# Kernel optimization log

Hardware: AMD Instinct MI355X
Metric: run time of the kernel (lower is better)

The kernel has to match this reference:

```python
import jax, jax.numpy as jnp
import numpy as np


def _xcorr3x3_valid(x, k):
    # x: [B,H,W], k: [B,3,3] per-sample kernel; cross-correlation (matches F.conv2d), VALID padding
    B, H, W = x.shape
    out = jnp.zeros((B, H - 2, W - 2), dtype=x.dtype)
    for u in range(3):
        for v in range(3):
            out = out + x[:, u:u + H - 2, v:v + W - 2] * k[:, u, v, None, None]
    return out


def setup_inputs() -> dict:
    key = jax.random.key(0)
    ks = jax.random.split(key, 4)
    B, H, W = 256, 256, 256
    pred = jax.random.normal(ks[0], (B, H, W), dtype=jnp.float32)
    rhs = jax.random.normal(ks[1], (B, H - 2, W - 2), dtype=jnp.float32)
    Laplace_kernel = jax.random.normal(ks[2], (B, 3, 3), dtype=jnp.float32)
    Df_dr_kernel = jax.random.normal(ks[3], (B, 3, 3), dtype=jnp.float32)
    # physically sensible meshgrids: R in [1,2] (avoids div-by-zero), Z in [-1,1]
    r = jnp.linspace(1.0, 2.0, W, dtype=jnp.float32)
    z = jnp.linspace(-1.0, 1.0, H, dtype=jnp.float32)
    RR = jnp.broadcast_to(r[None, None, :], (B, H, W)).astype(jnp.float32)
    ZZ = jnp.broadcast_to(z[None, :, None], (B, H, W)).astype(jnp.float32)
    Gauss_kernel = (jnp.array([[1., 2., 1.], [2., 4., 2.], [1., 2., 1.]], dtype=jnp.float32) / 16.0)
    return {"pred": pred, "rhs": rhs, "Laplace_kernel": Laplace_kernel,
            "Df_dr_kernel": Df_dr_kernel, "RR": RR, "ZZ": ZZ, "Gauss_kernel": Gauss_kernel}


def reference(pred, rhs, Laplace_kernel, Df_dr_kernel, RR, ZZ, Gauss_kernel):
    # Lpsi, Dpsi_dr: per-sample 3x3 VALID stencils -> [B, H-2, W-2]
    Lpsi = _xcorr3x3_valid(pred, Laplace_kernel)
    Dpsi_dr = -_xcorr3x3_valid(pred, Df_dr_kernel)
    Dpsi_dr = Dpsi_dr / RR[:, 1:-1, 1:-1]
    lhs = Lpsi - Dpsi_dr
    hr = (RR[:, 1, 2] - RR[:, 1, 1])[:, None, None]
    hz = (ZZ[:, 2, 1] - ZZ[:, 1, 1])[:, None, None]
    alfa = -2.0 * (hr ** 2 + hz ** 2)
    GS_ope = lhs * alfa / (hr ** 2 * hz ** 2)
    # Gaussian smoothing, shared kernel, SAME padding (cross-correlation; kernel is symmetric)
    sm = jax.lax.conv_general_dilated(
        GS_ope[:, None, :, :], Gauss_kernel[None, None, :, :],
        window_strides=(1, 1), padding='SAME')
    GS_ope_smooth = -sm
    rhs_computed = -GS_ope_smooth[:, 0, :, :]
    return jnp.mean((rhs_computed - rhs) ** 2)
```

## Files before the change

### kernel.cpp

```cpp
#include <hip/hip_runtime.h>


__global__ __launch_bounds__(256)
void pde_loss_kernel(const float* __restrict__ pred,
                     const float* __restrict__ rhs,
                     const float* __restrict__ KL,
                     const float* __restrict__ KD,
                     const float* __restrict__ RR,
                     const float* __restrict__ ZZ,
                     float* __restrict__ partials)
{
    constexpr int H = 256, W = 256, OH = 254, OW = 254, SR = 8;
    const int tid = threadIdx.x;
    const int l   = tid & 63;
    const int wv  = tid >> 6;
    const int b   = blockIdx.x >> 3;
    const int strip = (blockIdx.x & 7) * 4 + wv;
    const int o0 = strip * SR;
    const int o1 = (o0 + SR < OH) ? (o0 + SR) : OH;

    const size_t ib = (size_t)b * H * W;
    const float* predb = pred + ib;
    const float* rhsb  = rhs + (size_t)b * OH * OW;
    const int c0 = 4 * l;

    float4 p[12];
#pragma unroll
    for (int j = 0; j < 12; ++j) {
        const int row = o0 - 1 + j;
        p[j] = make_float4(0.f, 0.f, 0.f, 0.f);
        if ((unsigned)row < (unsigned)H)
            p[j] = *(const float4*)(predb + (size_t)row * W + c0);
    }
    float2 r0[8], r1[8];
#pragma unroll
    for (int j = 0; j < 8; ++j) {
        r0[j] = make_float2(0.f, 0.f); r1[j] = make_float2(0.f, 0.f);
        if (o0 + j < o1) {
            const float* rr = rhsb + (size_t)(o0 + j) * OW + c0;
            r0[j] = *(const float2*)rr;
            if (c0 + 2 < OW) r1[j] = *(const float2*)(rr + 2);
        }
    }

    const float hr  = RR[ib + W + 2] - RR[ib + W + 1];
    const float hz  = ZZ[ib + 2 * W + 1] - ZZ[ib + W + 1];
    float kl[9], kd[9];
#pragma unroll
    for (int t = 0; t < 9; ++t) {
        kl[t] = __int_as_float(__builtin_amdgcn_readfirstlane(__float_as_int(KL[b * 9 + t])));
        kd[t] = __int_as_float(__builtin_amdgcn_readfirstlane(__float_as_int(KD[b * 9 + t])));
    }
    float4 invr;
    invr.x = 1.0f / RR[ib + W + (c0 + 1)];
    invr.y = 1.0f / RR[ib + W + (c0 + 2)];
    invr.z = 1.0f / RR[ib + W + (c0 + 3)];
    invr.w = 1.0f / RR[ib + W + ((c0 + 4 < W) ? (c0 + 4) : (W - 1))];

    __builtin_amdgcn_sched_barrier(0);

    const float hr2 = hr * hr, hz2 = hz * hz;
    const float s   = -2.0f * (hr2 + hz2) / (hr2 * hz2);

    const float mzw = (l == 63) ? 0.f : 1.f;
    const float m23 = (c0 + 2 < OW) ? 1.f : 0.f;
    const float m0  = (l > 0) ? 1.f : 0.f;
    float4 s4, sir4;
    s4.x = s; s4.y = s; s4.z = s * mzw; s4.w = s * mzw;
    sir4.x = s4.x * invr.x; sir4.y = s4.y * invr.y;
    sir4.z = s4.z * invr.z; sir4.w = s4.w * invr.w;

#define SROW(SV, P, nx, ny, k0, k1, k2, KC)                                   \
    SV.x = fmaf(P.x, KC[k0], fmaf(P.y, KC[k1], fmaf(P.z, KC[k2], SV.x)));     \
    SV.y = fmaf(P.y, KC[k0], fmaf(P.z, KC[k1], fmaf(P.w, KC[k2], SV.y)));     \
    SV.z = fmaf(P.z, KC[k0], fmaf(P.w, KC[k1], fmaf(nx,  KC[k2], SV.z)));     \
    SV.w = fmaf(P.w, KC[k0], fmaf(nx,  KC[k1], fmaf(ny,  KC[k2], SV.w)));

    float ax = __shfl(p[0].x, l + 1, 64), ay = __shfl(p[0].y, l + 1, 64);
    float bx = __shfl(p[1].x, l + 1, 64), by = __shfl(p[1].y, l + 1, 64);
    float4 ghm2 = make_float4(0.f, 0.f, 0.f, 0.f);
    float4 ghm1 = make_float4(0.f, 0.f, 0.f, 0.f);
    float acc = 0.0f;

#pragma unroll
    for (int K = 0; K < 10; ++K) {
        const int g = o0 - 1 + K;

        const float cx = __shfl(p[K + 2].x, l + 1, 64);
        const float cy = __shfl(p[K + 2].y, l + 1, 64);

        float4 SL = make_float4(0.f, 0.f, 0.f, 0.f);
        float4 SD = make_float4(0.f, 0.f, 0.f, 0.f);
        if (g <= o1 && (unsigned)g < (unsigned)OH) {
            SROW(SL, p[K],     ax, ay, 0, 1, 2, kl)
            SROW(SL, p[K + 1], bx, by, 3, 4, 5, kl)
            SROW(SL, p[K + 2], cx, cy, 6, 7, 8, kl)
            SROW(SD, p[K],     ax, ay, 0, 1, 2, kd)
            SROW(SD, p[K + 1], bx, by, 3, 4, 5, kd)
            SROW(SD, p[K + 2], cx, cy, 6, 7, 8, kd)
        }
        float4 gs;
        gs.x = fmaf(s4.x, SL.x, sir4.x * SD.x);
        gs.y = fmaf(s4.y, SL.y, sir4.y * SD.y);
        gs.z = fmaf(s4.z, SL.z, sir4.z * SD.z);
        gs.w = fmaf(s4.w, SL.w, sir4.w * SD.w);

        const float up = __shfl(gs.w, l - 1, 64) * m0;
        const float dn = __shfl(gs.x, l + 1, 64);
        float4 gh;
        gh.x = fmaf(2.f, gs.x, up   + gs.y);
        gh.y = fmaf(2.f, gs.y, gs.x + gs.z);
        gh.z = fmaf(2.f, gs.z, gs.y + gs.w);
        gh.w = fmaf(2.f, gs.w, gs.z + dn);

        if (K >= 2) {
            const int i = g - 1;
            if (i < o1) {
                const float smx = (ghm2.x + 2.f * ghm1.x + gh.x) * 0.0625f;
                const float smy = (ghm2.y + 2.f * ghm1.y + gh.y) * 0.0625f;
                const float smz = (ghm2.z + 2.f * ghm1.z + gh.z) * 0.0625f;
                const float smw = (ghm2.w + 2.f * ghm1.w + gh.w) * 0.0625f;
                const float dx = smx - r0[K - 2].x;
                const float dy = smy - r0[K - 2].y;
                const float dz = (smz - r1[K - 2].x) * m23;
                const float dw = (smw - r1[K - 2].y) * m23;
                acc = fmaf(dx, dx, acc);
                acc = fmaf(dy, dy, acc);
                acc = fmaf(dz, dz, acc);
                acc = fmaf(dw, dw, acc);
            }
        }

        ghm2 = ghm1; ghm1 = gh;
        ax = bx; ay = by; bx = cx; by = cy;
    }
#undef SROW

#pragma unroll
    for (int off = 32; off > 0; off >>= 1)
        acc += __shfl_down(acc, off, 64);
    __shared__ float wsum[4];
    if (l == 0) wsum[wv] = acc;
    __syncthreads();
    if (tid == 0)
        partials[blockIdx.x] = (wsum[0] + wsum[1]) + (wsum[2] + wsum[3]);
}

__global__ __launch_bounds__(256)
void reduce_kernel(const float* __restrict__ partials, float* __restrict__ out,
                   int n, float inv_n)
{
    const int tid = threadIdx.x;
    float a = 0.0f;
    for (int i = tid; i < n; i += 256) a += partials[i];
#pragma unroll
    for (int off = 32; off > 0; off >>= 1)
        a += __shfl_down(a, off, 64);
    __shared__ float w[4];
    if ((tid & 63) == 0) w[tid >> 6] = a;
    __syncthreads();
    if (tid == 0) out[0] = ((w[0] + w[1]) + (w[2] + w[3])) * inv_n;
}

extern "C" void kernel_launch(void* const* d_in, const int* in_sizes, int n_in,
                              void* d_out, int out_size, void* d_ws, size_t ws_size,
                              hipStream_t stream) {
    const float* pred = (const float*)d_in[0];
    const float* rhs  = (const float*)d_in[1];
    const float* KL   = (const float*)d_in[2];
    const float* KD   = (const float*)d_in[3];
    const float* RR   = (const float*)d_in[4];
    const float* ZZ   = (const float*)d_in[5];
    float* out = (float*)d_out;

    const int B = in_sizes[2] / 9;
    const int nblocks = B * 8;
    const float inv_n = 1.0f / ((float)B * 254.0f * 254.0f);

    float* partials = (float*)d_ws;
    pde_loss_kernel<<<dim3(nblocks), dim3(256), 0, stream>>>(
        pred, rhs, KL, KD, RR, ZZ, partials);
    reduce_kernel<<<dim3(1), dim3(256), 0, stream>>>(partials, out, nblocks, inv_n);
}
```

Baseline: 221.1 us.

## Stage pred rows in LDS via direct global-to-LDS loads and fold stencil coefficients

Pred rows for the block are now loaded straight into shared memory with global_load_lds, and each wave reads its 12 rows from LDS. The right-halo columns come from an extra float2 LDS read, which replaces the cross-lane shuffles. The two per-sample stencils are also folded into one combined per-column coefficient set (klv*s + kdv*s/r). That halves the FMAs in the inner loop. The cost is a 37KB LDS footprint per block, which limits occupancy, plus a block barrier. The per-lane kernel coefficients also lose their scalar readfirstlane form and now occupy more VGPRs.

```diff
diff --git a/kernel.cpp b/kernel.cpp
--- a/kernel.cpp
+++ b/kernel.cpp
@@ -1,5 +1,12 @@
 #include <hip/hip_runtime.h>
 
+
+__device__ __forceinline__ void g2lds16(const float* g, float* l) {
+    __builtin_amdgcn_global_load_lds(
+        (const __attribute__((address_space(1))) void*)g,
+        (__attribute__((address_space(3))) void*)l,
+        16 , 0, 0);
+}
 
 __global__ __launch_bounds__(256)
 void pde_loss_kernel(const float* __restrict__ pred,
@@ -10,28 +17,23 @@
                      const float* __restrict__ ZZ,
                      float* __restrict__ partials)
 {
-    constexpr int H = 256, W = 256, OH = 254, OW = 254, SR = 8;
+    constexpr int H = 256, W = 256, OH = 254, OW = 254;
+    __shared__ float lds[36 * 256 + 16];
+    __shared__ float wsum[4];
+
     const int tid = threadIdx.x;
     const int l   = tid & 63;
     const int wv  = tid >> 6;
     const int b   = blockIdx.x >> 3;
-    const int strip = (blockIdx.x & 7) * 4 + wv;
-    const int o0 = strip * SR;
-    const int o1 = (o0 + SR < OH) ? (o0 + SR) : OH;
+    const int rb  = (blockIdx.x & 7) * 32;
+    const int o0  = rb + wv * 8;
+    const int o1  = (o0 + 8 < OH) ? (o0 + 8) : OH;
+    const int c0  = 4 * l;
 
     const size_t ib = (size_t)b * H * W;
     const float* predb = pred + ib;
     const float* rhsb  = rhs + (size_t)b * OH * OW;
-    const int c0 = 4 * l;
 
-    float4 p[12];
-#pragma unroll
-    for (int j = 0; j < 12; ++j) {
-        const int row = o0 - 1 + j;
-        p[j] = make_float4(0.f, 0.f, 0.f, 0.f);
-        if ((unsigned)row < (unsigned)H)
-            p[j] = *(const float4*)(predb + (size_t)row * W + c0);
-    }
     float2 r0[8], r1[8];
 #pragma unroll
     for (int j = 0; j < 8; ++j) {
@@ -42,68 +44,78 @@
             if (c0 + 2 < OW) r1[j] = *(const float2*)(rr + 2);
         }
     }
+    const float hr = RR[ib + W + 2] - RR[ib + W + 1];
+    const float hz = ZZ[ib + 2 * W + 1] - ZZ[ib + W + 1];
+    float klv[9], kdv[9];
+#pragma unroll
+    for (int t = 0; t < 9; ++t) { klv[t] = KL[b * 9 + t]; kdv[t] = KD[b * 9 + t]; }
+    float4 invr;
+    invr.x = RR[ib + W + (c0 + 1)];
+    invr.y = RR[ib + W + (c0 + 2)];
+    invr.z = RR[ib + W + (c0 + 3)];
+    invr.w = RR[ib + W + ((c0 + 4 < W) ? (c0 + 4) : (W - 1))];
 
-    const float hr  = RR[ib + W + 2] - RR[ib + W + 1];
-    const float hz  = ZZ[ib + 2 * W + 1] - ZZ[ib + W + 1];
-    float kl[9], kd[9];
 #pragma unroll
     for (int t = 0; t < 9; ++t) {
-        kl[t] = __int_as_float(__builtin_amdgcn_readfirstlane(__float_as_int(KL[b * 9 + t])));
-        kd[t] = __int_as_float(__builtin_amdgcn_readfirstlane(__float_as_int(KD[b * 9 + t])));
+        const int j  = wv + 4 * t;
+        const int gr = rb - 1 + j;
+        if ((unsigned)gr < (unsigned)H)
+            g2lds16(predb + (size_t)gr * W + c0, &lds[j * 256]);
     }
-    float4 invr;
-    invr.x = 1.0f / RR[ib + W + (c0 + 1)];
-    invr.y = 1.0f / RR[ib + W + (c0 + 2)];
-    invr.z = 1.0f / RR[ib + W + (c0 + 3)];
-    invr.w = 1.0f / RR[ib + W + ((c0 + 4 < W) ? (c0 + 4) : (W - 1))];
-
-    __builtin_amdgcn_sched_barrier(0);
 
     const float hr2 = hr * hr, hz2 = hz * hz;
     const float s   = -2.0f * (hr2 + hz2) / (hr2 * hz2);
-
-    const float mzw = (l == 63) ? 0.f : 1.f;
+    invr.x = 1.0f / invr.x; invr.y = 1.0f / invr.y;
+    invr.z = 1.0f / invr.z; invr.w = 1.0f / invr.w;
+    const bool lastl = (l == 63);
+    float4 c4[9];
+#pragma unroll
+    for (int t = 0; t < 9; ++t) {
+        const float a = klv[t] * s, d = kdv[t] * s;
+        c4[t].x = fmaf(d, invr.x, a);
+        c4[t].y = fmaf(d, invr.y, a);
+        c4[t].z = lastl ? 0.f : fmaf(d, invr.z, a);
+        c4[t].w = lastl ? 0.f : fmaf(d, invr.w, a);
+    }
     const float m23 = (c0 + 2 < OW) ? 1.f : 0.f;
     const float m0  = (l > 0) ? 1.f : 0.f;
-    float4 s4, sir4;
-    s4.x = s; s4.y = s; s4.z = s * mzw; s4.w = s * mzw;
-    sir4.x = s4.x * invr.x; sir4.y = s4.y * invr.y;
-    sir4.z = s4.z * invr.z; sir4.w = s4.w * invr.w;
 
-#define SROW(SV, P, nx, ny, k0, k1, k2, KC)                                   \
-    SV.x = fmaf(P.x, KC[k0], fmaf(P.y, KC[k1], fmaf(P.z, KC[k2], SV.x)));     \
-    SV.y = fmaf(P.y, KC[k0], fmaf(P.z, KC[k1], fmaf(P.w, KC[k2], SV.y)));     \
-    SV.z = fmaf(P.z, KC[k0], fmaf(P.w, KC[k1], fmaf(nx,  KC[k2], SV.z)));     \
-    SV.w = fmaf(P.w, KC[k0], fmaf(nx,  KC[k1], fmaf(ny,  KC[k2], SV.w)));
+    __syncthreads();
 
-    float ax = __shfl(p[0].x, l + 1, 64), ay = __shfl(p[0].y, l + 1, 64);
-    float bx = __shfl(p[1].x, l + 1, 64), by = __shfl(p[1].y, l + 1, 64);
+    const float* ldsw = &lds[wv * 8 * 256];
+    float4 p0 = *(const float4*)&ldsw[0 * 256 + c0];
+    float4 p1 = *(const float4*)&ldsw[1 * 256 + c0];
+    float4 p2 = *(const float4*)&ldsw[2 * 256 + c0];
+    float2 h0 = *(const float2*)&ldsw[0 * 256 + c0 + 4];
+    float2 h1 = *(const float2*)&ldsw[1 * 256 + c0 + 4];
+    float2 h2 = *(const float2*)&ldsw[2 * 256 + c0 + 4];
+
     float4 ghm2 = make_float4(0.f, 0.f, 0.f, 0.f);
     float4 ghm1 = make_float4(0.f, 0.f, 0.f, 0.f);
     float acc = 0.0f;
 
+#define SROW(P, Hh, t0, t1, t2)                                               \
+    gs.x = fmaf(P.x, c4[t0].x, fmaf(P.y, c4[t1].x, fmaf(P.z,  c4[t2].x, gs.x))); \
+    gs.y = fmaf(P.y, c4[t0].y, fmaf(P.z, c4[t1].y, fmaf(P.w,  c4[t2].y, gs.y))); \
+    gs.z = fmaf(P.z, c4[t0].z, fmaf(P.w, c4[t1].z, fmaf(Hh.x, c4[t2].z, gs.z))); \
+    gs.w = fmaf(P.w, c4[t0].w, fmaf(Hh.x, c4[t1].w, fmaf(Hh.y, c4[t2].w, gs.w)));
+
 #pragma unroll
     for (int K = 0; K < 10; ++K) {
+        float4 pr = make_float4(0.f, 0.f, 0.f, 0.f);
+        float2 hp = make_float2(0.f, 0.f);
+        if (K < 9) {
+            pr = *(const float4*)&ldsw[(K + 3) * 256 + c0];
+            hp = *(const float2*)&ldsw[(K + 3) * 256 + c0 + 4];
+        }
+
         const int g = o0 - 1 + K;
-
-        const float cx = __shfl(p[K + 2].x, l + 1, 64);
-        const float cy = __shfl(p[K + 2].y, l + 1, 64);
-
-        float4 SL = make_float4(0.f, 0.f, 0.f, 0.f);
-        float4 SD = make_float4(0.f, 0.f, 0.f, 0.f);
+        float4 gs = make_float4(0.f, 0.f, 0.f, 0.f);
         if (g <= o1 && (unsigned)g < (unsigned)OH) {
-            SROW(SL, p[K],     ax, ay, 0, 1, 2, kl)
-            SROW(SL, p[K + 1], bx, by, 3, 4, 5, kl)
-            SROW(SL, p[K + 2], cx, cy, 6, 7, 8, kl)
-            SROW(SD, p[K],     ax, ay, 0, 1, 2, kd)
-            SROW(SD, p[K + 1], bx, by, 3, 4, 5, kd)
-            SROW(SD, p[K + 2], cx, cy, 6, 7, 8, kd)
+            SROW(p0, h0, 0, 1, 2)
+            SROW(p1, h1, 3, 4, 5)
+            SROW(p2, h2, 6, 7, 8)
         }
-        float4 gs;
-        gs.x = fmaf(s4.x, SL.x, sir4.x * SD.x);
-        gs.y = fmaf(s4.y, SL.y, sir4.y * SD.y);
-        gs.z = fmaf(s4.z, SL.z, sir4.z * SD.z);
-        gs.w = fmaf(s4.w, SL.w, sir4.w * SD.w);
 
         const float up = __shfl(gs.w, l - 1, 64) * m0;
         const float dn = __shfl(gs.x, l + 1, 64);
@@ -131,15 +143,15 @@
             }
         }
 
+        p0 = p1; p1 = p2; p2 = pr;
+        h0 = h1; h1 = h2; h2 = hp;
         ghm2 = ghm1; ghm1 = gh;
-        ax = bx; ay = by; bx = cx; by = cy;
     }
 #undef SROW
 
 #pragma unroll
     for (int off = 32; off > 0; off >>= 1)
         acc += __shfl_down(acc, off, 64);
-    __shared__ float wsum[4];
     if (l == 0) wsum[wv] = acc;
     __syncthreads();
     if (tid == 0)
```

Result: faster. 213.5 us (-3.4%).
